# Kernel optimization log

Measured on AMD Instinct MI355X. Metric: run time of the kernel, lower is better.

The kernel has to match this reference:

```python
import jax, jax.numpy as jnp
import numpy as np

N, D, H, E = 4096, 512, 8, 131072
DH = D // H
EPS = 1e-5
NEG = -1e9


def layer_norm(x, w, b):
    m = jnp.mean(x, axis=-1, keepdims=True)
    v = jnp.mean((x - m) ** 2, axis=-1, keepdims=True)
    return (x - m) * jax.lax.rsqrt(v + EPS) * w + b


def setup_inputs() -> dict:
    key = jax.random.key(0)
    ks = jax.random.split(key, 10)
    s = 0.02
    return {
        "x": jax.random.normal(ks[0], (N, D), dtype=jnp.float32),
        "edge_index": jax.random.randint(ks[1], (2, E), 0, N, dtype=jnp.int64),
        "ln1_w": jnp.ones((D,), jnp.float32),
        "ln1_b": jnp.zeros((D,), jnp.float32),
        "w_in": jax.random.normal(ks[2], (3 * D, D), jnp.float32) * s,
        "b_in": jnp.zeros((3 * D,), jnp.float32),
        "w_out": jax.random.normal(ks[3], (D, D), jnp.float32) * s,
        "b_out": jnp.zeros((D,), jnp.float32),
        "ln2_w": jnp.ones((D,), jnp.float32),
        "ln2_b": jnp.zeros((D,), jnp.float32),
        "w1": jax.random.normal(ks[4], (4 * D, D), jnp.float32) * s,
        "b1": jnp.zeros((4 * D,), jnp.float32),
        "w2": jax.random.normal(ks[5], (D, 4 * D), jnp.float32) * s,
        "b2": jnp.zeros((D,), jnp.float32),
    }


def reference(x, edge_index, ln1_w, ln1_b, w_in, b_in, w_out, b_out,
              ln2_w, ln2_b, w1, b1, w2, b2):
    n = x.shape[0]
    # adjacency mask: allowed where edge exists or on diagonal
    adj = jnp.zeros((n, n), dtype=bool)
    adj = adj.at[edge_index[0], edge_index[1]].set(True)
    adj = adj.at[jnp.arange(n), jnp.arange(n)].set(True)
    add_mask = jnp.where(adj, 0.0, NEG).astype(x.dtype)  # [n, n]

    xn = layer_norm(x, ln1_w, ln1_b)
    qkv = xn @ w_in.T + b_in  # [n, 3D]
    q, k, v = jnp.split(qkv, 3, axis=-1)
    # [n, D] -> [H, n, DH]
    q = q.reshape(n, H, DH).transpose(1, 0, 2)
    k = k.reshape(n, H, DH).transpose(1, 0, 2)
    v = v.reshape(n, H, DH).transpose(1, 0, 2)
    scores = jnp.einsum("hqd,hkd->hqk", q, k) / jnp.sqrt(jnp.asarray(DH, x.dtype))
    scores = scores + add_mask[None]
    attn = jax.nn.softmax(scores, axis=-1)
    o = jnp.einsum("hqk,hkd->hqd", attn, v)  # [H, n, DH]
    o = o.transpose(1, 0, 2).reshape(n, D)
    attn_out = o @ w_out.T + b_out

    x = x + attn_out  # residual (dropout=0 / eval)
    xm = layer_norm(x, ln2_w, ln2_b)
    mlp = jax.nn.relu(xm @ w1.T + b1) @ w2.T + b2
    return x + mlp
```

## Files before the change

kernel.cpp:

```cpp
#include <hip/hip_runtime.h>

#define NN 4096
#define DD 512
#define HH 8
#define DHH 64

typedef __attribute__((ext_vector_type(8))) __bf16 bfrag;
typedef __attribute__((ext_vector_type(8))) short short8;
typedef __attribute__((ext_vector_type(8))) unsigned short ushort8v;
typedef __attribute__((ext_vector_type(4))) float f32x4;
typedef unsigned int uint32;

#define GLOAD16(gp, lp)                                                        \
    __builtin_amdgcn_global_load_lds(                                          \
        (const __attribute__((address_space(1))) unsigned int*)(gp),           \
        (__attribute__((address_space(3))) unsigned int*)(lp), 16, 0, 0)

template <int N>
__device__ __forceinline__ void waitcnt_vm() {
    if constexpr (N == 0) asm volatile("s_waitcnt vmcnt(0)" ::: "memory");
    else if constexpr (N == 4) asm volatile("s_waitcnt vmcnt(4)" ::: "memory");
    else if constexpr (N == 6) asm volatile("s_waitcnt vmcnt(6)" ::: "memory");
    else if constexpr (N == 8) asm volatile("s_waitcnt vmcnt(8)" ::: "memory");
    else if constexpr (N == 12) asm volatile("s_waitcnt vmcnt(12)" ::: "memory");
    else static_assert(N == 0, "unsupported vmcnt literal");
}

__device__ __forceinline__ unsigned short f2b(float f) {
    unsigned int u = __builtin_bit_cast(unsigned int, f);
    unsigned int r = 0x7fffu + ((u >> 16) & 1u);
    return (unsigned short)((u + r) >> 16);
}

__device__ __forceinline__ float b2f(unsigned short u) {
    return __builtin_bit_cast(float, (unsigned int)u << 16);
}

__device__ __forceinline__ float fexp2(float x) {
#if __has_builtin(__builtin_amdgcn_exp2f)
    return __builtin_amdgcn_exp2f(x);
#else
    return exp2f(x);
#endif
}

__device__ __forceinline__ void load_edge(const void* ei, int E, int i, int is32,
                                          int& r, int& c) {
    if (is32) {
        const int* p = (const int*)ei;
        r = p[i]; c = p[E + i];
    } else {
        const long long* p = (const long long*)ei;
        r = (int)p[i]; c = (int)p[E + i];
    }
}

__device__ __forceinline__ void ln_row_wave(const float* __restrict__ x,
                                            const float* __restrict__ w,
                                            const float* __restrict__ b,
                                            unsigned short* __restrict__ out,
                                            int row, int lane) {
    const float4* xp = reinterpret_cast<const float4*>(x + (size_t)row * DD + lane * 8);
    const float4 v0 = xp[0], v1 = xp[1];
    float s  = (v0.x + v0.y) + (v0.z + v0.w) + (v1.x + v1.y) + (v1.z + v1.w);
    float s2 = v0.x * v0.x + v0.y * v0.y + v0.z * v0.z + v0.w * v0.w +
               v1.x * v1.x + v1.y * v1.y + v1.z * v1.z + v1.w * v1.w;
#pragma unroll
    for (int d = 1; d < 64; d <<= 1) {
        s += __shfl_xor(s, d);
        s2 += __shfl_xor(s2, d);
    }
    const float mean = s * (1.f / DD);
    const float var = fmaxf(s2 * (1.f / DD) - mean * mean, 0.f);
    const float rs = rsqrtf(var + 1e-5f);
    const float4* wp = reinterpret_cast<const float4*>(w + lane * 8);
    const float4* bp = reinterpret_cast<const float4*>(b + lane * 8);
    const float4 w0 = wp[0], w1 = wp[1], b0 = bp[0], b1 = bp[1];
    ushort8v o;
    o[0] = f2b((v0.x - mean) * rs * w0.x + b0.x);
    o[1] = f2b((v0.y - mean) * rs * w0.y + b0.y);
    o[2] = f2b((v0.z - mean) * rs * w0.z + b0.z);
    o[3] = f2b((v0.w - mean) * rs * w0.w + b0.w);
    o[4] = f2b((v1.x - mean) * rs * w1.x + b1.x);
    o[5] = f2b((v1.y - mean) * rs * w1.y + b1.y);
    o[6] = f2b((v1.z - mean) * rs * w1.z + b1.z);
    o[7] = f2b((v1.w - mean) * rs * w1.w + b1.w);
    *reinterpret_cast<ushort8v*>(out + (size_t)row * DD + lane * 8) = o;
}

__global__ __launch_bounds__(256) void ln_rows(const float* __restrict__ x,
                                               const float* __restrict__ w,
                                               const float* __restrict__ b,
                                               unsigned short* __restrict__ out) {
    ln_row_wave(x, w, b, out, blockIdx.x * 4 + (threadIdx.x >> 6), threadIdx.x & 63);
}

#define W_IN_N 786432
#define W_OUT_N 262144
#define W1_N 1048576
#define W2_N 1048576
#define CVT_BLKS 3072
#define LN_BLKS 1024
__global__ __launch_bounds__(256) void prologue(
    const float* __restrict__ w_in, const float* __restrict__ w_out,
    const float* __restrict__ w1, const float* __restrict__ w2,
    unsigned short* __restrict__ o_in, unsigned short* __restrict__ o_out,
    unsigned short* __restrict__ o1, unsigned short* __restrict__ o2,
    const float* __restrict__ x, const float* __restrict__ ln1w,
    const float* __restrict__ ln1b, unsigned short* __restrict__ xn,
    const void* __restrict__ ei, uint32* __restrict__ mask, int E) {
    const int bb = blockIdx.x;
    if (bb < CVT_BLKS) {
        int idx = (bb * 256 + threadIdx.x) * 4;
        const float* src;
        unsigned short* dst;
        int off;
        if (idx < W_IN_N) { src = w_in; dst = o_in; off = idx; }
        else if (idx < W_IN_N + W_OUT_N) { src = w_out; dst = o_out; off = idx - W_IN_N; }
        else if (idx < W_IN_N + W_OUT_N + W1_N) { src = w1; dst = o1; off = idx - (W_IN_N + W_OUT_N); }
        else { src = w2; dst = o2; off = idx - (W_IN_N + W_OUT_N + W1_N); }
        float4 v = *reinterpret_cast<const float4*>(src + off);
        ushort4 o;
        o.x = f2b(v.x); o.y = f2b(v.y); o.z = f2b(v.z); o.w = f2b(v.w);
        *reinterpret_cast<ushort4*>(dst + off) = o;
    } else if (bb < CVT_BLKS + LN_BLKS) {
        ln_row_wave(x, ln1w, ln1b, xn,
                    (bb - CVT_BLKS) * 4 + (threadIdx.x >> 6), threadIdx.x & 63);
    } else {
        __shared__ int s_any;
        if (threadIdx.x == 0) s_any = 0;
        __syncthreads();
        if (((const int*)ei)[2 * threadIdx.x + 1] != 0) atomicOr(&s_any, 1);
        __syncthreads();
        const int is32 = s_any;
        const int tid = (bb - (CVT_BLKS + LN_BLKS)) * 256 + threadIdx.x;
        const int total = E + NN;
        if (tid < total) {
            int r, c;
            if (tid < E) load_edge(ei, E, tid, is32, r, c);
            else { r = tid - E; c = r; }
            atomicOr(&mask[r * 128 + (c >> 5)], 1u << (c & 31));
        }
    }
}

template <int BM, int BN, int EPI, int PD>
__global__ __launch_bounds__(256) void gemm_swz(const unsigned short* __restrict__ A,
                                                const unsigned short* __restrict__ B,
                                                int K,
                                                const float* __restrict__ bias,
                                                const float* __restrict__ resid,
                                                float* __restrict__ out_f,
                                                unsigned short* __restrict__ out_b,
                                                unsigned short* __restrict__ q_out,
                                                unsigned short* __restrict__ k_out,
                                                unsigned short* __restrict__ v_out) {
    constexpr int MR = BM / 32;
    constexpr int NR = BN / 32;
    constexpr int LA = BM / 32;
    constexpr int LB = BN / 32;
    constexpr int CSTR = BN + 4;
    constexpr size_t PIPE_B = (size_t)PD * (BM + BN) * 64 * 2;
    constexpr size_t EPI_B = (size_t)BM * CSTR * 4;
    constexpr size_t LDS_B = PIPE_B > EPI_B ? PIPE_B : EPI_B;
    __shared__ __align__(16) unsigned char smem[LDS_B];
    unsigned short* a_lds = (unsigned short*)smem;
    unsigned short* b_lds = a_lds + (size_t)PD * BM * 64;
    float* c_lds = (float*)smem;

    const int tid = threadIdx.x;
    const int lane = tid & 63;
    const int wave = tid >> 6;
    const int wm = wave >> 1, wn = wave & 1;
    const int wgid = blockIdx.x;
    const int tm = wgid % (NN / BM);
    const int tn = wgid / (NN / BM);

    f32x4 acc[MR][NR];
#pragma unroll
    for (int mi = 0; mi < MR; ++mi)
#pragma unroll
        for (int ni = 0; ni < NR; ++ni) acc[mi][ni] = (f32x4){0.f, 0.f, 0.f, 0.f};

    const int srow = lane >> 3;
    const int sswz = ((lane & 7) ^ srow) << 3;
    const unsigned short* a_src = A + (size_t)(tm * BM + srow) * K + sswz;
    const unsigned short* b_src = B + (size_t)(tn * BN + srow) * K + sswz;

    auto stage = [&](int k0, int buf) {
        unsigned short* al = a_lds + buf * (BM * 64);
        unsigned short* bl = b_lds + buf * (BN * 64);
#pragma unroll
        for (int i = 0; i < LA; ++i) {
            const int c = wave * LA + i;
            GLOAD16(a_src + (size_t)c * 8 * K + k0, al + c * 512);
        }
#pragma unroll
        for (int i = 0; i < LB; ++i) {
            const int c = wave * LB + i;
            GLOAD16(b_src + (size_t)c * 8 * K + k0, bl + c * 512);
        }
    };

    const int NT = K >> 6;
    stage(0, 0);
    if constexpr (PD == 3) stage(64, 1);
    for (int t = 0; t < NT; ++t) {
        const int cur = t % PD;
        if (t + PD - 1 < NT) {
            stage((t + PD - 1) << 6, (t + PD - 1) % PD);
            waitcnt_vm<(PD - 1) * (LA + LB)>();
        } else if (PD == 3 && t + 1 < NT) {
            waitcnt_vm<LA + LB>();
        } else {
            waitcnt_vm<0>();
        }
        __builtin_amdgcn_s_barrier();
        asm volatile("" ::: "memory");
        const unsigned short* al = a_lds + cur * (BM * 64);
        const unsigned short* bl = b_lds + cur * (BN * 64);
#pragma unroll
        for (int ks = 0; ks < 2; ++ks) {
            const int cswz = (((lane >> 4) + ks * 4) ^ (lane & 7)) << 3;
            const int rl = lane & 15;
            bfrag af[MR], bfr[NR];
#pragma unroll
            for (int mi = 0; mi < MR; ++mi)
                af[mi] = *reinterpret_cast<const bfrag*>(
                    &al[(wm * (BM / 2) + mi * 16 + rl) * 64 + cswz]);
#pragma unroll
            for (int ni = 0; ni < NR; ++ni)
                bfr[ni] = *reinterpret_cast<const bfrag*>(
                    &bl[(wn * (BN / 2) + ni * 16 + rl) * 64 + cswz]);
#pragma unroll
            for (int mi = 0; mi < MR; ++mi)
#pragma unroll
                for (int ni = 0; ni < NR; ++ni)
                    acc[mi][ni] = __builtin_amdgcn_mfma_f32_16x16x32_bf16(
                        af[mi], bfr[ni], acc[mi][ni], 0, 0, 0);
        }
        asm volatile("" ::: "memory");
        __builtin_amdgcn_s_barrier();
    }

    __syncthreads();
    {
        const int r0 = (lane >> 4) << 2;
        const int cl = lane & 15;
        float bias_r[NR];
#pragma unroll
        for (int ni = 0; ni < NR; ++ni)
            bias_r[ni] = bias[tn * BN + wn * (BN / 2) + ni * 16 + cl];
#pragma unroll
        for (int mi = 0; mi < MR; ++mi)
#pragma unroll
            for (int ni = 0; ni < NR; ++ni) {
                const int row_l = wm * (BM / 2) + mi * 16 + r0;
                const int col_l = wn * (BN / 2) + ni * 16 + cl;
#pragma unroll
                for (int r = 0; r < 4; ++r)
                    c_lds[(size_t)(row_l + r) * CSTR + col_l] =
                        acc[mi][ni][r] + bias_r[ni];
            }
    }
    __syncthreads();

    if constexpr (EPI == 1) {
        constexpr int IT = (BM * BN) / 1024;
#pragma unroll
        for (int it = 0; it < IT; ++it) {
            const int seg = tid + it * 256;
            const int row = seg / (BN / 4);
            const int c4 = (seg % (BN / 4)) * 4;
            f32x4 v = *reinterpret_cast<const f32x4*>(&c_lds[(size_t)row * CSTR + c4]);
            const size_t gidx = (size_t)(tm * BM + row) * 512 + tn * BN + c4;
            f32x4 rs = *reinterpret_cast<const f32x4*>(&resid[gidx]);
            *reinterpret_cast<f32x4*>(&out_f[gidx]) = v + rs;
        }
    } else {
        constexpr int IT = (BM * BN) / 2048;
        unsigned short* dst;
        int cbase, stride;
        float scl = 1.f;
        if constexpr (EPI == 0) {
            const int gc0 = tn * BN;
            const int region = gc0 >> 9;
            dst = region == 0 ? q_out : (region == 1 ? k_out : v_out);
            cbase = gc0 - region * 512;
            stride = 512;
            if (region == 0) scl = 0.18033688011112042f;
        } else {
            dst = out_b;
            cbase = tn * BN;
            stride = 2048;
        }
#pragma unroll
        for (int it = 0; it < IT; ++it) {
            const int seg = tid + it * 256;
            const int row = seg / (BN / 8);
            const int c8 = (seg % (BN / 8)) * 8;
            f32x4 v0 = *reinterpret_cast<const f32x4*>(&c_lds[(size_t)row * CSTR + c8]);
            f32x4 v1 = *reinterpret_cast<const f32x4*>(&c_lds[(size_t)row * CSTR + c8 + 4]);
            ushort8v o;
            if constexpr (EPI == 0) {
#pragma unroll
                for (int i = 0; i < 4; ++i) o[i] = f2b(v0[i] * scl);
#pragma unroll
                for (int i = 0; i < 4; ++i) o[4 + i] = f2b(v1[i] * scl);
            } else {
#pragma unroll
                for (int i = 0; i < 4; ++i) o[i] = f2b(fmaxf(v0[i], 0.f));
#pragma unroll
                for (int i = 0; i < 4; ++i) o[4 + i] = f2b(fmaxf(v1[i], 0.f));
            }
            *reinterpret_cast<ushort8v*>(
                dst + (size_t)(tm * BM + row) * stride + cbase + c8) = o;
        }
    }
}

__global__ __launch_bounds__(256) void attn_sparse(const unsigned short* __restrict__ qb,
                                                   const unsigned short* __restrict__ kb,
                                                   const unsigned short* __restrict__ vb,
                                                   const uint32* __restrict__ mask,
                                                   unsigned short* __restrict__ o_buf) {
    __shared__ int s_cols[4][1024];
    __shared__ int s_cnt[4];
    const int lane = threadIdx.x & 63;
    const int wid = threadIdx.x >> 6;
    const int q = blockIdx.x * 4 + wid;

    if (lane == 0) s_cnt[wid] = 0;
    uint32 w0 = mask[q * 128 + lane];
    uint32 w1 = mask[q * 128 + 64 + lane];
    const int base0 = lane * 32, base1 = (64 + lane) * 32;
    while (w0) {
        int b = __builtin_ctz(w0);
        w0 &= w0 - 1;
        int pos = atomicAdd(&s_cnt[wid], 1);
        s_cols[wid][pos & 1023] = base0 + b;
    }
    while (w1) {
        int b = __builtin_ctz(w1);
        w1 &= w1 - 1;
        int pos = atomicAdd(&s_cnt[wid], 1);
        s_cols[wid][pos & 1023] = base1 + b;
    }
    const int cnt = min(s_cnt[wid], 1024);

    ushort8v q8 = *reinterpret_cast<const ushort8v*>(qb + (size_t)q * DD + lane * 8);
    float qf[8];
#pragma unroll
    for (int i = 0; i < 8; ++i) qf[i] = b2f(q8[i]);

    float m_run = -3.0e38f, l_run = 0.f;
    float oa[8];
#pragma unroll
    for (int i = 0; i < 8; ++i) oa[i] = 0.f;

    for (int j0 = 0; j0 < cnt; j0 += 8) {
        float s_arr[8];
        int col_arr[8];
#pragma unroll
        for (int u = 0; u < 8; ++u) {
            const int idx = j0 + u;
            const bool act = idx < cnt;
            const int col = s_cols[wid][act ? idx : 0];
            col_arr[u] = col;
            ushort8v kq = *reinterpret_cast<const ushort8v*>(
                kb + (size_t)col * DD + lane * 8);
            float d = qf[0] * b2f(kq[0]);
            d = fmaf(qf[1], b2f(kq[1]), d);
            d = fmaf(qf[2], b2f(kq[2]), d);
            d = fmaf(qf[3], b2f(kq[3]), d);
            d = fmaf(qf[4], b2f(kq[4]), d);
            d = fmaf(qf[5], b2f(kq[5]), d);
            d = fmaf(qf[6], b2f(kq[6]), d);
            d = fmaf(qf[7], b2f(kq[7]), d);
            d += __shfl_xor(d, 1);
            d += __shfl_xor(d, 2);
            d += __shfl_xor(d, 4);
            s_arr[u] = act ? d : -3.0e38f;
        }
        float mloc = fmaxf(fmaxf(fmaxf(s_arr[0], s_arr[1]), fmaxf(s_arr[2], s_arr[3])),
                           fmaxf(fmaxf(s_arr[4], s_arr[5]), fmaxf(s_arr[6], s_arr[7])));
        if (mloc > m_run) {
            const float alpha = fexp2(m_run - mloc);
            l_run *= alpha;
#pragma unroll
            for (int i = 0; i < 8; ++i) oa[i] *= alpha;
            m_run = mloc;
        }
#pragma unroll
        for (int u = 0; u < 8; ++u) {
            const float p = fexp2(s_arr[u] - m_run);
            l_run += p;
            ushort8v vq = *reinterpret_cast<const ushort8v*>(
                vb + (size_t)col_arr[u] * DD + lane * 8);
#pragma unroll
            for (int i = 0; i < 8; ++i) oa[i] = fmaf(p, b2f(vq[i]), oa[i]);
        }
    }

    const float rl = 1.f / l_run;
    ushort8v ov;
#pragma unroll
    for (int i = 0; i < 8; ++i) ov[i] = f2b(oa[i] * rl);
    *reinterpret_cast<ushort8v*>(o_buf + (size_t)q * DD + lane * 8) = ov;
}

extern "C" void kernel_launch(void* const* d_in, const int* in_sizes, int n_in,
                              void* d_out, int out_size, void* d_ws, size_t ws_size,
                              hipStream_t stream) {
    const float* x = (const float*)d_in[0];
    const void* ei = d_in[1];
    const float* ln1w = (const float*)d_in[2];
    const float* ln1b = (const float*)d_in[3];
    const float* w_in = (const float*)d_in[4];
    const float* b_in = (const float*)d_in[5];
    const float* w_out = (const float*)d_in[6];
    const float* b_out = (const float*)d_in[7];
    const float* ln2w = (const float*)d_in[8];
    const float* ln2b = (const float*)d_in[9];
    const float* w1 = (const float*)d_in[10];
    const float* b1 = (const float*)d_in[11];
    const float* w2 = (const float*)d_in[12];
    const float* b2 = (const float*)d_in[13];
    float* out = (float*)d_out;
    const int E = in_sizes[1] / 2;

    char* ws = (char*)d_ws;
    size_t off = 0;
    auto alloc = [&](size_t bytes) -> void* {
        void* p = ws + off;
        off = (off + bytes + 255) & ~(size_t)255;
        return p;
    };
    uint32* mask1 = (uint32*)alloc((size_t)NN * 128 * 4);
    unsigned short* w_in_b = (unsigned short*)alloc((size_t)1536 * 512 * 2);
    unsigned short* w_out_b = (unsigned short*)alloc((size_t)512 * 512 * 2);
    unsigned short* w1_b = (unsigned short*)alloc((size_t)2048 * 512 * 2);
    unsigned short* w2_b = (unsigned short*)alloc((size_t)512 * 2048 * 2);
    unsigned short* xn = (unsigned short*)alloc((size_t)NN * DD * 2);
    unsigned short* q_b = (unsigned short*)alloc((size_t)NN * DD * 2);
    unsigned short* k_b = (unsigned short*)alloc((size_t)NN * DD * 2);
    unsigned short* v_b = (unsigned short*)alloc((size_t)NN * DD * 2);
    unsigned short* o_buf = (unsigned short*)alloc((size_t)NN * DD * 2);
    float* x1 = (float*)alloc((size_t)NN * DD * 4);
    unsigned short* xm = (unsigned short*)alloc((size_t)NN * DD * 2);
    unsigned short* h_buf = q_b;

    hipMemsetAsync(mask1, 0, (size_t)NN * 128 * 4, stream);

    const int adj_blks = (E + NN + 255) / 256;
    prologue<<<CVT_BLKS + LN_BLKS + adj_blks, 256, 0, stream>>>(
        w_in, w_out, w1, w2, w_in_b, w_out_b, w1_b, w2_b,
        x, ln1w, ln1b, xn, ei, mask1, E);

    gemm_swz<128, 64, 0, 2><<<32 * 24, 256, 0, stream>>>(
        xn, w_in_b, 512, b_in, nullptr, nullptr, nullptr, q_b, k_b, v_b);
    attn_sparse<<<NN / 4, 256, 0, stream>>>(q_b, k_b, v_b, mask1, o_buf);
    gemm_swz<64, 64, 1, 3><<<64 * 8, 256, 0, stream>>>(
        o_buf, w_out_b, 512, b_out, x, x1, nullptr, nullptr, nullptr, nullptr);
    ln_rows<<<NN / 4, 256, 0, stream>>>(x1, ln2w, ln2b, xm);
    gemm_swz<128, 128, 2, 2><<<32 * 16, 256, 0, stream>>>(
        xm, w1_b, 512, b1, nullptr, nullptr, h_buf, nullptr, nullptr, nullptr);
    gemm_swz<64, 64, 1, 3><<<64 * 8, 256, 0, stream>>>(
        h_buf, w2_b, 2048, b2, x1, out, nullptr, nullptr, nullptr, nullptr);
}
```

Baseline: 97.75 us.

## Load GEMM B operand directly into registers instead of staging through LDS

The GEMM kernel now stages only the A tile through LDS, double-buffered. Each wave reads its own B fragments straight from global memory into registers, with two register buffers for prefetch. The aim is to cut LDS traffic and capacity for B and raise occupancy. The cost is redundant global reads of B across waves that share columns, more registers, and the loss of the 3-stage pipeline previously used for the 64x64 GEMMs.

```diff
diff --git a/kernel.cpp b/kernel.cpp
--- a/kernel.cpp
+++ b/kernel.cpp
@@ -19,7 +19,6 @@
 template <int N>
 __device__ __forceinline__ void waitcnt_vm() {
     if constexpr (N == 0) asm volatile("s_waitcnt vmcnt(0)" ::: "memory");
-    else if constexpr (N == 4) asm volatile("s_waitcnt vmcnt(4)" ::: "memory");
     else if constexpr (N == 6) asm volatile("s_waitcnt vmcnt(6)" ::: "memory");
     else if constexpr (N == 8) asm volatile("s_waitcnt vmcnt(8)" ::: "memory");
     else if constexpr (N == 12) asm volatile("s_waitcnt vmcnt(12)" ::: "memory");
@@ -144,7 +143,7 @@
     }
 }
 
-template <int BM, int BN, int EPI, int PD>
+template <int BM, int BN, int EPI>
 __global__ __launch_bounds__(256) void gemm_swz(const unsigned short* __restrict__ A,
                                                 const unsigned short* __restrict__ B,
                                                 int K,
@@ -158,14 +157,13 @@
     constexpr int MR = BM / 32;
     constexpr int NR = BN / 32;
     constexpr int LA = BM / 32;
-    constexpr int LB = BN / 32;
+    constexpr int BATCH = LA + 2 * NR;
     constexpr int CSTR = BN + 4;
-    constexpr size_t PIPE_B = (size_t)PD * (BM + BN) * 64 * 2;
+    constexpr size_t PIPE_B = (size_t)2 * BM * 64 * 2;
     constexpr size_t EPI_B = (size_t)BM * CSTR * 4;
     constexpr size_t LDS_B = PIPE_B > EPI_B ? PIPE_B : EPI_B;
     __shared__ __align__(16) unsigned char smem[LDS_B];
     unsigned short* a_lds = (unsigned short*)smem;
-    unsigned short* b_lds = a_lds + (size_t)PD * BM * 64;
     float* c_lds = (float*)smem;
 
     const int tid = threadIdx.x;
@@ -185,62 +183,80 @@
     const int srow = lane >> 3;
     const int sswz = ((lane & 7) ^ srow) << 3;
     const unsigned short* a_src = A + (size_t)(tm * BM + srow) * K + sswz;
-    const unsigned short* b_src = B + (size_t)(tn * BN + srow) * K + sswz;
 
     auto stage = [&](int k0, int buf) {
         unsigned short* al = a_lds + buf * (BM * 64);
-        unsigned short* bl = b_lds + buf * (BN * 64);
 #pragma unroll
         for (int i = 0; i < LA; ++i) {
             const int c = wave * LA + i;
             GLOAD16(a_src + (size_t)c * 8 * K + k0, al + c * 512);
         }
-#pragma unroll
-        for (int i = 0; i < LB; ++i) {
-            const int c = wave * LB + i;
-            GLOAD16(b_src + (size_t)c * 8 * K + k0, bl + c * 512);
-        }
     };
 
-    const int NT = K >> 6;
-    stage(0, 0);
-    if constexpr (PD == 3) stage(64, 1);
-    for (int t = 0; t < NT; ++t) {
-        const int cur = t % PD;
-        if (t + PD - 1 < NT) {
-            stage((t + PD - 1) << 6, (t + PD - 1) % PD);
-            waitcnt_vm<(PD - 1) * (LA + LB)>();
-        } else if (PD == 3 && t + 1 < NT) {
-            waitcnt_vm<LA + LB>();
-        } else {
-            waitcnt_vm<0>();
-        }
-        __builtin_amdgcn_s_barrier();
-        asm volatile("" ::: "memory");
-        const unsigned short* al = a_lds + cur * (BM * 64);
-        const unsigned short* bl = b_lds + cur * (BN * 64);
+    const unsigned short* bptr[NR];
+#pragma unroll
+    for (int ni = 0; ni < NR; ++ni)
+        bptr[ni] = B + (size_t)(tn * BN + wn * (BN / 2) + ni * 16 + (lane & 15)) * K +
+                   ((lane >> 4) << 3);
+
+    bfrag sB0[NR][2], sB1[NR][2];
+    auto load_b = [&](int k0, bfrag (&dst)[NR][2]) {
+#pragma unroll
+        for (int ni = 0; ni < NR; ++ni)
+#pragma unroll
+            for (int ks = 0; ks < 2; ++ks)
+                dst[ni][ks] = *reinterpret_cast<const bfrag*>(bptr[ni] + k0 + ks * 32);
+    };
+
+    const int rl = lane & 15;
+    auto compute = [&](const unsigned short* al, bfrag (&bs)[NR][2]) {
 #pragma unroll
         for (int ks = 0; ks < 2; ++ks) {
             const int cswz = (((lane >> 4) + ks * 4) ^ (lane & 7)) << 3;
-            const int rl = lane & 15;
-            bfrag af[MR], bfr[NR];
+            bfrag af[MR];
 #pragma unroll
             for (int mi = 0; mi < MR; ++mi)
                 af[mi] = *reinterpret_cast<const bfrag*>(
                     &al[(wm * (BM / 2) + mi * 16 + rl) * 64 + cswz]);
 #pragma unroll
-            for (int ni = 0; ni < NR; ++ni)
-                bfr[ni] = *reinterpret_cast<const bfrag*>(
-                    &bl[(wn * (BN / 2) + ni * 16 + rl) * 64 + cswz]);
-#pragma unroll
             for (int mi = 0; mi < MR; ++mi)
 #pragma unroll
                 for (int ni = 0; ni < NR; ++ni)
                     acc[mi][ni] = __builtin_amdgcn_mfma_f32_16x16x32_bf16(
-                        af[mi], bfr[ni], acc[mi][ni], 0, 0, 0);
-        }
+                        af[mi], bs[ni][ks], acc[mi][ni], 0, 0, 0);
+        }
+    };
+
+    const int NT = K >> 6;
+    stage(0, 0);
+    load_b(0, sB0);
+    for (int t = 0; t < NT; t += 2) {
+        if (t + 1 < NT) {
+            stage((t + 1) << 6, 1);
+            load_b((t + 1) << 6, sB1);
+            waitcnt_vm<BATCH>();
+        } else {
+            waitcnt_vm<0>();
+        }
+        __builtin_amdgcn_s_barrier();
+        asm volatile("" ::: "memory");
+        compute(a_lds, sB0);
         asm volatile("" ::: "memory");
         __builtin_amdgcn_s_barrier();
+        if (t + 1 < NT) {
+            if (t + 2 < NT) {
+                stage((t + 2) << 6, 0);
+                load_b((t + 2) << 6, sB0);
+                waitcnt_vm<BATCH>();
+            } else {
+                waitcnt_vm<0>();
+            }
+            __builtin_amdgcn_s_barrier();
+            asm volatile("" ::: "memory");
+            compute(a_lds + BM * 64, sB1);
+            asm volatile("" ::: "memory");
+            __builtin_amdgcn_s_barrier();
+        }
     }
 
     __syncthreads();
@@ -457,14 +473,14 @@
         w_in, w_out, w1, w2, w_in_b, w_out_b, w1_b, w2_b,
         x, ln1w, ln1b, xn, ei, mask1, E);
 
-    gemm_swz<128, 64, 0, 2><<<32 * 24, 256, 0, stream>>>(
+    gemm_swz<128, 64, 0><<<32 * 24, 256, 0, stream>>>(
         xn, w_in_b, 512, b_in, nullptr, nullptr, nullptr, q_b, k_b, v_b);
     attn_sparse<<<NN / 4, 256, 0, stream>>>(q_b, k_b, v_b, mask1, o_buf);
-    gemm_swz<64, 64, 1, 3><<<64 * 8, 256, 0, stream>>>(
+    gemm_swz<64, 64, 1><<<64 * 8, 256, 0, stream>>>(
         o_buf, w_out_b, 512, b_out, x, x1, nullptr, nullptr, nullptr, nullptr);
     ln_rows<<<NN / 4, 256, 0, stream>>>(x1, ln2w, ln2b, xm);
-    gemm_swz<128, 128, 2, 2><<<32 * 16, 256, 0, stream>>>(
+    gemm_swz<128, 128, 2><<<32 * 16, 256, 0, stream>>>(
         xm, w1_b, 512, b1, nullptr, nullptr, h_buf, nullptr, nullptr, nullptr);
-    gemm_swz<64, 64, 1, 3><<<64 * 8, 256, 0, stream>>>(
+    gemm_swz<64, 64, 1><<<64 * 8, 256, 0, stream>>>(
         h_buf, w2_b, 2048, b2, x1, out, nullptr, nullptr, nullptr, nullptr);
 }
```

Result: slower. 137.0 us (+40.2%).
